# Kernel tuning notes

Measured on AMD Instinct MI355X. Metric: run time of the kernel, lower is better.

## Reference

```python
import jax, jax.numpy as jnp
import numpy as np

BETA = 0.9
GAMMA = -0.1
EPSILON = 1.1
EPS = 1e-08

NUM_INPUTS = 8
NUM_OUTPUTS = 8
UNITS = 256
BATCH = 8192


def setup_inputs() -> dict:
    key = jax.random.key(0)
    k_x, k_a, k_u, k_t = jax.random.split(key, 4)
    x_stack = jax.random.normal(k_x, (BATCH, NUM_INPUTS, UNITS), dtype=jnp.float32)
    alpha = jax.random.uniform(k_a, (1,), dtype=jnp.float32)  # torch.rand(1)
    u_param = jax.random.uniform(k_u, (NUM_OUTPUTS, NUM_INPUTS), dtype=jnp.float32,
                                 minval=EPS, maxval=1.0 - EPS)
    # xavier_normal_ on [o, n, u, u]: fan_in = n*u*u? torch: fan_out = o*u*u, fan_in = n*u*u
    fan_in = NUM_INPUTS * UNITS * UNITS
    fan_out = NUM_OUTPUTS * UNITS * UNITS
    std = float(np.sqrt(2.0 / (fan_in + fan_out)))
    trans_matrix = std * jax.random.normal(k_t, (NUM_OUTPUTS, NUM_INPUTS, UNITS, UNITS),
                                           dtype=jnp.float32)
    return {"x_stack": x_stack, "alpha": alpha, "u_param": u_param,
            "trans_matrix": trans_matrix}


def reference(x_stack, alpha, u_param, trans_matrix):
    # Hard-concrete style gate: s = sigmoid(logit(u) + log(alpha)/beta)
    s = jax.nn.sigmoid(jnp.log(u_param) - jnp.log(1.0 - u_param)
                       + jnp.log(alpha) / BETA)          # [o, n]
    z = jnp.clip(s * (EPSILON - GAMMA) + GAMMA, 0.0, 1.0)  # [o, n]
    # Fused gated grouped matmul + reduction over inputs n:
    # equivalent to einsum('bnu,onuv->bonv') * z[None,:,:,None] summed over n.
    out = jnp.einsum('bnu,onuv,on->bov', x_stack, trans_matrix, z)  # [b, o, v]
    return out
```

## Files before the change

### kernel.cpp

```cpp
#include <hip/hip_runtime.h>
#include <hip/hip_bf16.h>

#define BATCH 8192
#define KDIM  2048
#define NDIM  2048

typedef short bf16x8 __attribute__((ext_vector_type(8)));
typedef float f32x4  __attribute__((ext_vector_type(4)));

__device__ __forceinline__ unsigned short f2bf(float f) {
    unsigned int u = __float_as_uint(f);
    u = u + 0x7fffu + ((u >> 16) & 1u);
    return (unsigned short)(u >> 16);
}

__global__ __launch_bounds__(256) void pack_a(const float* __restrict__ x,
                                              short* __restrict__ a) {
    int h = blockIdx.x * 256 + threadIdx.x;
    const f32x4* xv = (const f32x4*)x;
    f32x4 v0 = xv[(size_t)h * 2];
    f32x4 v1 = xv[(size_t)h * 2 + 1];
    bf16x8 r;
    r[0] = (short)f2bf(v0[0]); r[1] = (short)f2bf(v0[1]);
    r[2] = (short)f2bf(v0[2]); r[3] = (short)f2bf(v0[3]);
    r[4] = (short)f2bf(v1[0]); r[5] = (short)f2bf(v1[1]);
    r[6] = (short)f2bf(v1[2]); r[7] = (short)f2bf(v1[3]);
    ((bf16x8*)a)[h] = r;
}

__global__ __launch_bounds__(256) void pack_b(const float* __restrict__ T,
                                              const float* __restrict__ u_param,
                                              const float* __restrict__ alpha,
                                              short* __restrict__ bp) {
    __shared__ short tl[256 * 33];
    int bid = blockIdx.x;
    int o  = bid >> 6;
    int n  = (bid >> 3) & 7;
    int v0 = (bid & 7) * 32;
    int tid = threadIdx.x;

    float up = u_param[o * 8 + n];
    float t  = logf(up) - logf(1.0f - up) + logf(alpha[0]) * (1.0f / 0.9f);
    float s  = 1.0f / (1.0f + expf(-t));
    float z  = fminf(fmaxf(s * 1.2f - 0.1f, 0.0f), 1.0f);

    const f32x4* T4 = (const f32x4*)(T + ((size_t)(o * 8 + n) << 16));
#pragma unroll
    for (int it = 0; it < 8; ++it) {
        int f = it * 256 + tid;
        int u = f >> 3, vv = (f & 7) * 4;
        f32x4 val = T4[(u * 256 + v0 + vv) >> 2];
#pragma unroll
        for (int j = 0; j < 4; ++j)
            tl[u * 33 + vv + j] = (short)f2bf(z * val[j]);
    }
    __syncthreads();
#pragma unroll
    for (int it = 0; it < 4; ++it) {
        int g = it * 256 + tid;
        int v = g >> 5, ch = g & 31;
        bf16x8 r;
#pragma unroll
        for (int q = 0; q < 8; ++q) r[q] = tl[(ch * 8 + q) * 33 + v];
        *(bf16x8*)&bp[(size_t)(o * 256 + v0 + v) * KDIM + n * 256 + ch * 8] = r;
    }
}

#define SBAR() do { __builtin_amdgcn_sched_barrier(0); \
                    __builtin_amdgcn_s_barrier(); \
                    __builtin_amdgcn_sched_barrier(0); } while (0)

#define MMQ(q) do { \
    __builtin_amdgcn_s_setprio(1); \
    _Pragma("unroll") for (int mm = 0; mm < 2; ++mm) \
    _Pragma("unroll") for (int nn = 0; nn < 4; ++nn) \
    _Pragma("unroll") for (int k8 = 0; k8 < 2; ++k8) \
        acc[(q)*2 + mm][nn] = __builtin_amdgcn_mfma_f32_16x16x32_bf16( \
            afr[mm][k8], bfr[nn][k8], acc[(q)*2 + mm][nn], 0, 0, 0); \
    __builtin_amdgcn_s_setprio(0); \
} while (0)

__global__ __launch_bounds__(512, 2) void gemm(const short* __restrict__ A,
                                               const short* __restrict__ B,
                                               float* __restrict__ C) {
    __shared__ __align__(16) short lds[65536];

    const int tid  = threadIdx.x;
    const int lane = tid & 63;
    const int wid  = tid >> 6;
    const int wr = wid >> 2, wc = wid & 3;
    const int l15 = lane & 15, hi8 = (lane >> 4) * 8;
    const int sx  = (lane & 7) << 3;

    int bid = blockIdx.x;
    int wg  = (bid & 7) * 32 + (bid >> 3);
    int by = wg >> 3, bx = wg & 7;
    const int bm = by * 256, bn = bx * 256;

    int r_[2], c_[2];
#pragma unroll
    for (int i = 0; i < 2; ++i) {
        int L = i * 4096 + tid * 8;
        int S = L ^ (((L >> 6) & 7) << 3);
        r_[i] = S >> 6; c_[i] = S & 63;
    }

    auto stA = [&](int buf, int h, int kt) {
#pragma unroll
        for (int i = 0; i < 2; ++i) {
            const short* src = A + (size_t)(bm + h * 128 + r_[i]) * KDIM + kt * 64 + c_[i];
            __builtin_amdgcn_global_load_lds(
                (const __attribute__((address_space(1))) void*)src,
                (__attribute__((address_space(3))) void*)&lds[buf * 16384 + h * 8192 + i * 4096 + tid * 8],
                16, 0, 0);
        }
    };
    auto stB = [&](int buf, int h, int kt) {
#pragma unroll
        for (int i = 0; i < 2; ++i) {
            const short* src = B + (size_t)(bn + h * 128 + r_[i]) * KDIM + kt * 64 + c_[i];
            __builtin_amdgcn_global_load_lds(
                (const __attribute__((address_space(1))) void*)src,
                (__attribute__((address_space(3))) void*)&lds[32768 + buf * 16384 + h * 8192 + i * 4096 + tid * 8],
                16, 0, 0);
        }
    };

    f32x4  acc[8][4] = {};
    bf16x8 bfr[4][2];
    bf16x8 afr[2][2];

    auto rdB = [&](int buf) {
        int base = 32768 + buf * 16384 + (wc * 64 + l15) * 64 + hi8;
#pragma unroll
        for (int nn = 0; nn < 4; ++nn)
#pragma unroll
            for (int k8 = 0; k8 < 2; ++k8)
                bfr[nn][k8] = *(const bf16x8*)&lds[(base + nn * 1024 + k8 * 32) ^ sx];
    };
    auto rdA = [&](int buf, int q) {
        int base = buf * 16384 + (wr * 128 + q * 32 + l15) * 64 + hi8;
#pragma unroll
        for (int mm = 0; mm < 2; ++mm)
#pragma unroll
            for (int k8 = 0; k8 < 2; ++k8)
                afr[mm][k8] = *(const bf16x8*)&lds[(base + mm * 1024 + k8 * 32) ^ sx];
    };

    stA(0, 0, 0); stA(0, 1, 0);
    stB(0, 0, 0); stB(0, 1, 0);
    stB(1, 0, 1); stB(1, 1, 1);
    asm volatile("s_waitcnt vmcnt(4)" ::: "memory");
    SBAR();

    for (int i = 0; i < 16; ++i) {
        int t1 = 2 * i + 1, t2 = (2 * i + 2) & 31, t3 = (2 * i + 3) & 31;
        rdB(0); rdA(0, 0); stA(1, 0, t1);
        SBAR(); MMQ(0); SBAR();
        rdA(0, 1); stA(1, 1, t1);
        SBAR(); MMQ(1); SBAR();
        rdA(0, 2); stB(0, 0, t2);
        SBAR(); MMQ(2); SBAR();
        rdA(0, 3); stB(0, 1, t2);
        SBAR(); MMQ(3);
        asm volatile("s_waitcnt vmcnt(4)" ::: "memory");
        SBAR();
        rdB(1); rdA(1, 0); stA(0, 0, t2);
        SBAR(); MMQ(0); SBAR();
        rdA(1, 1); stA(0, 1, t2);
        SBAR(); MMQ(1); SBAR();
        rdA(1, 2); stB(1, 0, t3);
        SBAR(); MMQ(2); SBAR();
        rdA(1, 3); stB(1, 1, t3);
        SBAR(); MMQ(3);
        asm volatile("s_waitcnt vmcnt(4)" ::: "memory");
        SBAR();
    }
    asm volatile("s_waitcnt vmcnt(0)" ::: "memory");

    int r0 = bm + wr * 128 + (lane >> 4) * 4;
    int c0 = bn + wc * 64 + l15;
#pragma unroll
    for (int m = 0; m < 8; ++m)
#pragma unroll
        for (int nn = 0; nn < 4; ++nn)
#pragma unroll
            for (int r = 0; r < 4; ++r)
                C[(size_t)(r0 + m * 16 + r) * NDIM + c0 + nn * 16] = acc[m][nn][r];
}

extern "C" void kernel_launch(void* const* d_in, const int* in_sizes, int n_in,
                              void* d_out, int out_size, void* d_ws, size_t ws_size,
                              hipStream_t stream) {
    const float* x       = (const float*)d_in[0];
    const float* alpha   = (const float*)d_in[1];
    const float* u_param = (const float*)d_in[2];
    const float* T       = (const float*)d_in[3];
    float* out = (float*)d_out;

    short* Abf = (short*)d_ws;
    short* Bp  = (short*)((char*)d_ws + (size_t)BATCH * KDIM * 2);

    hipLaunchKernelGGL(pack_a, dim3((BATCH * KDIM / 8) / 256), dim3(256), 0, stream, x, Abf);
    hipLaunchKernelGGL(pack_b, dim3(512), dim3(256), 0, stream, T, u_param, alpha, Bp);
    hipLaunchKernelGGL(gemm, dim3((BATCH / 256) * (NDIM / 256)), dim3(512), 0, stream,
                       Abf, Bp, out);
}
```

Measured before the change: 186.8 us.

## Double-buffer A fragments in registers to overlap LDS reads with MFMA

Splits the A-fragment registers into two sets and issues the next quarter's LDS reads before running MFMAs on the current set. Partial lgkmcnt waits replace the full barrier that sat before each MFMA group. The aim is to hide LDS read latency behind matrix math and cut barriers per k-step. In exchange it uses more VGPRs, and the new wait counts must stay correct given that global_load_lds also touches the counters.

```diff
diff --git a/kernel.cpp b/kernel.cpp
--- a/kernel.cpp
+++ b/kernel.cpp
@@ -66,17 +66,32 @@
     }
 }
 
-#define SBAR() do { __builtin_amdgcn_sched_barrier(0); \
-                    __builtin_amdgcn_s_barrier(); \
-                    __builtin_amdgcn_sched_barrier(0); } while (0)
-
-#define MMQ(q) do { \
+#define SCB() __builtin_amdgcn_sched_barrier(0)
+#define BAR1() do { SCB(); __builtin_amdgcn_s_barrier(); SCB(); } while (0)
+#define WAITK(n) do { SCB(); asm volatile("s_waitcnt lgkmcnt(" #n ")" ::: "memory"); SCB(); } while (0)
+#define WAITV4() do { SCB(); asm volatile("s_waitcnt vmcnt(4)" ::: "memory"); SCB(); } while (0)
+
+#define LDB(buf) do { \
+    int base = 32768 + (buf) * 16384 + (wc * 64 + l15) * 64 + hi8; \
+    _Pragma("unroll") for (int nn = 0; nn < 4; ++nn) \
+    _Pragma("unroll") for (int k8 = 0; k8 < 2; ++k8) \
+        bfr[nn][k8] = *(const bf16x8*)&lds[(base + nn * 1024 + k8 * 32) ^ sx]; \
+} while (0)
+
+#define LDA(buf, q, SET) do { \
+    int base = (buf) * 16384 + (wr * 128 + (q) * 32 + l15) * 64 + hi8; \
+    _Pragma("unroll") for (int mm = 0; mm < 2; ++mm) \
+    _Pragma("unroll") for (int k8 = 0; k8 < 2; ++k8) \
+        SET[mm][k8] = *(const bf16x8*)&lds[(base + mm * 1024 + k8 * 32) ^ sx]; \
+} while (0)
+
+#define MM(q, SET) do { \
     __builtin_amdgcn_s_setprio(1); \
     _Pragma("unroll") for (int mm = 0; mm < 2; ++mm) \
     _Pragma("unroll") for (int nn = 0; nn < 4; ++nn) \
     _Pragma("unroll") for (int k8 = 0; k8 < 2; ++k8) \
         acc[(q)*2 + mm][nn] = __builtin_amdgcn_mfma_f32_16x16x32_bf16( \
-            afr[mm][k8], bfr[nn][k8], acc[(q)*2 + mm][nn], 0, 0, 0); \
+            SET[mm][k8], bfr[nn][k8], acc[(q)*2 + mm][nn], 0, 0, 0); \
     __builtin_amdgcn_s_setprio(0); \
 } while (0)
 
@@ -128,53 +143,38 @@
 
     f32x4  acc[8][4] = {};
     bf16x8 bfr[4][2];
-    bf16x8 afr[2][2];
-
-    auto rdB = [&](int buf) {
-        int base = 32768 + buf * 16384 + (wc * 64 + l15) * 64 + hi8;
-#pragma unroll
-        for (int nn = 0; nn < 4; ++nn)
-#pragma unroll
-            for (int k8 = 0; k8 < 2; ++k8)
-                bfr[nn][k8] = *(const bf16x8*)&lds[(base + nn * 1024 + k8 * 32) ^ sx];
-    };
-    auto rdA = [&](int buf, int q) {
-        int base = buf * 16384 + (wr * 128 + q * 32 + l15) * 64 + hi8;
-#pragma unroll
-        for (int mm = 0; mm < 2; ++mm)
-#pragma unroll
-            for (int k8 = 0; k8 < 2; ++k8)
-                afr[mm][k8] = *(const bf16x8*)&lds[(base + mm * 1024 + k8 * 32) ^ sx];
-    };
+    bf16x8 afrX[2][2], afrY[2][2];
 
     stA(0, 0, 0); stA(0, 1, 0);
     stB(0, 0, 0); stB(0, 1, 0);
     stB(1, 0, 1); stB(1, 1, 1);
-    asm volatile("s_waitcnt vmcnt(4)" ::: "memory");
-    SBAR();
+    WAITV4();
+    BAR1();
 
     for (int i = 0; i < 16; ++i) {
         int t1 = 2 * i + 1, t2 = (2 * i + 2) & 31, t3 = (2 * i + 3) & 31;
-        rdB(0); rdA(0, 0); stA(1, 0, t1);
-        SBAR(); MMQ(0); SBAR();
-        rdA(0, 1); stA(1, 1, t1);
-        SBAR(); MMQ(1); SBAR();
-        rdA(0, 2); stB(0, 0, t2);
-        SBAR(); MMQ(2); SBAR();
-        rdA(0, 3); stB(0, 1, t2);
-        SBAR(); MMQ(3);
-        asm volatile("s_waitcnt vmcnt(4)" ::: "memory");
-        SBAR();
-        rdB(1); rdA(1, 0); stA(0, 0, t2);
-        SBAR(); MMQ(0); SBAR();
-        rdA(1, 1); stA(0, 1, t2);
-        SBAR(); MMQ(1); SBAR();
-        rdA(1, 2); stB(1, 0, t3);
-        SBAR(); MMQ(2); SBAR();
-        rdA(1, 3); stB(1, 1, t3);
-        SBAR(); MMQ(3);
-        asm volatile("s_waitcnt vmcnt(4)" ::: "memory");
-        SBAR();
+        LDB(0); LDA(0, 0, afrX); stA(1, 0, t1);
+        SCB();
+        LDA(0, 1, afrY);
+        WAITK(4); MM(0, afrX); BAR1();
+        LDA(0, 2, afrX); stA(1, 1, t1);
+        WAITK(4); MM(1, afrY); BAR1();
+        LDA(0, 3, afrY); stB(0, 0, t2);
+        WAITK(4); MM(2, afrX); BAR1();
+        stB(0, 1, t2);
+        WAITK(0); MM(3, afrY);
+        WAITV4(); BAR1();
+        LDB(1); LDA(1, 0, afrX); stA(0, 0, t2);
+        SCB();
+        LDA(1, 1, afrY);
+        WAITK(4); MM(0, afrX); BAR1();
+        LDA(1, 2, afrX); stA(0, 1, t2);
+        WAITK(4); MM(1, afrY); BAR1();
+        LDA(1, 3, afrY); stB(1, 0, t3);
+        WAITK(4); MM(2, afrX); BAR1();
+        stB(1, 1, t3);
+        WAITK(0); MM(3, afrY);
+        WAITV4(); BAR1();
     }
     asm volatile("s_waitcnt vmcnt(0)" ::: "memory");
 
```

Result: slower. 209.9 us (+12.3%).
